# Kernel tuning notes

Measured on AMD Instinct MI355X. Metric: run time of the kernel, lower is better.

## Reference

```python
import jax, jax.numpy as jnp
import numpy as np

DIM = 1024
HEADS = 16
HEAD_DIM = DIM // HEADS
HIDDEN = 4 * DIM
EPS = 1e-5

def _layernorm(x, w, b):
    mu = jnp.mean(x, axis=-1, keepdims=True)
    var = jnp.mean(jnp.square(x - mu), axis=-1, keepdims=True)
    return (x - mu) * jax.lax.rsqrt(var + EPS) * w + b

def setup_inputs() -> dict:
    key = jax.random.key(0)
    ks = jax.random.split(key, 8)
    B, N, C = 4, 1024, DIM
    s = lambda fan_in: 1.0 / np.sqrt(fan_in)
    return {
        "x": jax.random.normal(ks[0], (B, N, C), dtype=jnp.float32),
        "ln1_w": jnp.ones((C,), jnp.float32),
        "ln1_b": jnp.zeros((C,), jnp.float32),
        "qkv_w": jax.random.normal(ks[1], (3 * C, C), jnp.float32) * s(C),
        "proj_w": jax.random.normal(ks[2], (C, C), jnp.float32) * s(C),
        "proj_b": jnp.zeros((C,), jnp.float32),
        "ln2_w": jnp.ones((C,), jnp.float32),
        "ln2_b": jnp.zeros((C,), jnp.float32),
        "fc1_w": jax.random.normal(ks[3], (HIDDEN, C), jnp.float32) * s(C),
        "fc1_b": jnp.zeros((HIDDEN,), jnp.float32),
        "fc2_w": jax.random.normal(ks[4], (C, HIDDEN), jnp.float32) * s(HIDDEN),
        "fc2_b": jnp.zeros((C,), jnp.float32),
    }

def reference(x, ln1_w, ln1_b, qkv_w, proj_w, proj_b, ln2_w, ln2_b, fc1_w, fc1_b, fc2_w, fc2_b):
    B, N, C = x.shape
    H, D = HEADS, HEAD_DIM
    scale = D ** -0.5
    # --- attention branch (pre-norm) ---
    h = _layernorm(x, ln1_w, ln1_b)
    qkv = jnp.einsum('bnc,oc->bno', h, qkv_w)          # [B,N,3C], no bias (qkv_bias=False)
    qkv = qkv.reshape(B, N, 3, H, D)
    q = jnp.transpose(qkv[:, :, 0], (0, 2, 1, 3))       # [B,H,N,D]
    k = jnp.transpose(qkv[:, :, 1], (0, 2, 1, 3))
    v = jnp.transpose(qkv[:, :, 2], (0, 2, 1, 3))
    attn = jnp.einsum('bhnd,bhmd->bhnm', q, k) * scale  # [B,H,N,N]
    attn = jax.nn.softmax(attn, axis=-1)
    o = jnp.einsum('bhnm,bhmd->bhnd', attn, v)          # [B,H,N,D]
    o = jnp.transpose(o, (0, 2, 1, 3)).reshape(B, N, C)
    o = jnp.einsum('bnc,oc->bno', o, proj_w) + proj_b
    x = x + o
    # --- MLP branch (pre-norm); drop=0.0 -> identity ---
    h = _layernorm(x, ln2_w, ln2_b)
    h = jnp.einsum('bnc,hc->bnh', h, fc1_w) + fc1_b
    h = jax.nn.gelu(h, approximate=False)               # nn.GELU exact erf form
    h = jnp.einsum('bnh,ch->bnc', h, fc2_w) + fc2_b
    return x + h
```

## Files before the change

### kernel.cpp

```cpp
#include <hip/hip_runtime.h>
#include <hip/hip_bf16.h>
#include <math.h>
#include <stdint.h>

#define SEQ 1024
#define CDIM 1024
#define NHEAD 16
#define HIDDEN 4096
#define BATCH 4
#define MROWS (BATCH*SEQ)

using bf16x8 = __attribute__((ext_vector_type(8))) short;
using f32x4  = __attribute__((ext_vector_type(4))) float;

__device__ __forceinline__ short f2bf(float f) {
    union { float f; uint32_t u; } c; c.f = f;
    const uint32_t u = c.u + 0x7FFFu + ((c.u >> 16) & 1u);
    return (short)(u >> 16);
}

__device__ __forceinline__ float gelu_exact(float v) {
    return 0.5f * v * (1.0f + erff(v * 0.70710678118654752440f));
}

__device__ __forceinline__ void gload_lds16(const short* g, short* lds) {
    __builtin_amdgcn_global_load_lds(
        (const __attribute__((address_space(1))) void*)(uintptr_t)g,
        (__attribute__((address_space(3))) void*)(uintptr_t)lds,
        16, 0, 0);
}

__global__ void cvt_bf16_kernel(const float* __restrict__ in, short* __restrict__ out) {
    const size_t i = ((size_t)blockIdx.x * 256 + threadIdx.x) * 8;
    const float4 a = *(const float4*)(in + i);
    const float4 b = *(const float4*)(in + i + 4);
    bf16x8 s;
    s[0] = f2bf(a.x); s[1] = f2bf(a.y); s[2] = f2bf(a.z); s[3] = f2bf(a.w);
    s[4] = f2bf(b.x); s[5] = f2bf(b.y); s[6] = f2bf(b.z); s[7] = f2bf(b.w);
    *(bf16x8*)(out + i) = s;
}

__global__ void ln_kernel(const float* __restrict__ x, const float* __restrict__ w,
                          const float* __restrict__ b, short* __restrict__ out) {
    const int row = blockIdx.x;
    const int t = threadIdx.x;
    const float4* xr = (const float4*)(x + (size_t)row * CDIM);
    float4 v = xr[t];
    float s  = v.x + v.y + v.z + v.w;
    float sq = v.x*v.x + v.y*v.y + v.z*v.z + v.w*v.w;
    #pragma unroll
    for (int off = 32; off; off >>= 1) {
        s  += __shfl_down(s, off);
        sq += __shfl_down(sq, off);
    }
    __shared__ float ss[4], ssq[4];
    const int wid = t >> 6, lane = t & 63;
    if (lane == 0) { ss[wid] = s; ssq[wid] = sq; }
    __syncthreads();
    s  = ss[0] + ss[1] + ss[2] + ss[3];
    sq = ssq[0] + ssq[1] + ssq[2] + ssq[3];
    const float mu  = s * (1.0f / CDIM);
    const float var = sq * (1.0f / CDIM) - mu * mu;
    const float rs  = rsqrtf(var + 1e-5f);
    const float4 wv = ((const float4*)w)[t];
    const float4 bv = ((const float4*)b)[t];
    short4 o;
    o.x = f2bf((v.x - mu) * rs * wv.x + bv.x);
    o.y = f2bf((v.y - mu) * rs * wv.y + bv.y);
    o.z = f2bf((v.z - mu) * rs * wv.z + bv.z);
    o.w = f2bf((v.w - mu) * rs * wv.w + bv.w);
    *(short4*)(out + (size_t)row * CDIM + t * 4) = o;
}

template<int BN, bool BIAS, bool RES, bool GELU_, bool OUTBF16>
__global__ __launch_bounds__(256) void mgemm(
    const short* __restrict__ A, const short* __restrict__ B,
    const float* __restrict__ bias, const float* __restrict__ res,
    void* __restrict__ Cv, int M, int N, int K)
{
    constexpr int MF = (BN == 128) ? 4 : 2;
    __shared__ __align__(16) short As[2][128 * 32];
    __shared__ __align__(16) short Bs[2][BN * 32];
    const int t = threadIdx.x;
    const int w = t >> 6, l = t & 63;

    const int gx = gridDim.x;
    const int nwg = gx * gridDim.y;
    const int lid = blockIdx.y * gx + blockIdx.x;
    const int swz = (lid & 7) * (nwg >> 3) + (lid >> 3);
    const int bx = swz % gx, by = swz / gx;
    const int m0 = by * 128, n0 = bx * BN;

    const int wrow = (BN == 128) ? (w >> 1) * 64 : w * 32;
    const int wcol = (BN == 128) ? (w & 1) * 64 : 0;

    const short* agp0 = A + (size_t)(m0 + w * 32 + (l >> 2)) * K + (l & 3) * 8;
    const short* agp1 = agp0 + (size_t)16 * K;
    const short* bgp0;
    const short* bgp1 = nullptr;
    if (BN == 128) {
        bgp0 = B + (size_t)(n0 + w * 32 + (l >> 2)) * K + (l & 3) * 8;
        bgp1 = bgp0 + (size_t)16 * K;
    } else {
        bgp0 = B + (size_t)(n0 + w * 16 + (l >> 2)) * K + (l & 3) * 8;
    }

    int aoff[MF], boff[4];
    #pragma unroll
    for (int m = 0; m < MF; ++m) aoff[m] = (wrow + m * 16 + (l & 15)) * 32 + (l >> 4) * 8;
    #pragma unroll
    for (int n = 0; n < 4; ++n)  boff[n] = (wcol + n * 16 + (l & 15)) * 32 + (l >> 4) * 8;

    auto stage = [&](int k0, int buf) {
        short* ldsA = &As[buf][w * 1024];
        gload_lds16(agp0 + k0, ldsA);
        gload_lds16(agp1 + k0, ldsA + 512);
        if (BN == 128) {
            short* ldsB = &Bs[buf][w * 1024];
            gload_lds16(bgp0 + k0, ldsB);
            gload_lds16(bgp1 + k0, ldsB + 512);
        } else {
            gload_lds16(bgp0 + k0, &Bs[buf][w * 512]);
        }
    };

    f32x4 acc[MF][4] = {};
    stage(0, 0);
    int cur = 0;
    for (int k0 = 0; k0 < K; k0 += 32) {
        __syncthreads();
        if (k0 + 32 < K) stage(k0 + 32, cur ^ 1);
        bf16x8 af[MF], bfr[4];
        #pragma unroll
        for (int m = 0; m < MF; ++m) af[m]  = *(const bf16x8*)&As[cur][aoff[m]];
        #pragma unroll
        for (int n = 0; n < 4; ++n)  bfr[n] = *(const bf16x8*)&Bs[cur][boff[n]];
        #pragma unroll
        for (int m = 0; m < MF; ++m)
            #pragma unroll
            for (int n = 0; n < 4; ++n)
                acc[m][n] = __builtin_amdgcn_mfma_f32_16x16x32_bf16(af[m], bfr[n], acc[m][n], 0, 0, 0);
        cur ^= 1;
    }

    const int lr4 = (l >> 4) * 4, lc = l & 15;
    #pragma unroll
    for (int m = 0; m < MF; ++m) {
        #pragma unroll
        for (int n = 0; n < 4; ++n) {
            const int col = n0 + wcol + n * 16 + lc;
            const float bv = BIAS ? bias[col] : 0.0f;
            #pragma unroll
            for (int r = 0; r < 4; ++r) {
                const int row = m0 + wrow + m * 16 + lr4 + r;
                float v = acc[m][n][r] + bv;
                if (GELU_) v = gelu_exact(v);
                if (RES)   v += res[(size_t)row * N + col];
                if (OUTBF16) ((short*)Cv)[(size_t)row * N + col] = f2bf(v);
                else         ((float*)Cv)[(size_t)row * N + col] = v;
            }
        }
    }
}

__global__ __launch_bounds__(256) void qkv_gemm(
    const short* __restrict__ A, const short* __restrict__ B,
    short* __restrict__ qkvb, short* __restrict__ VT, int K)
{
    __shared__ __align__(16) short As[2][128 * 32];
    __shared__ __align__(16) short Bs[2][128 * 32];
    const int t = threadIdx.x;
    const int w = t >> 6, l = t & 63;
    const int wr = w >> 1, wc = w & 1;

    const int gx = gridDim.x;
    const int nwg = gx * gridDim.y;
    const int lid = blockIdx.y * gx + blockIdx.x;
    const int swz = (lid & 7) * (nwg >> 3) + (lid >> 3);
    const int bx = swz % gx, by = swz / gx;
    const int m0 = by * 128, n0 = bx * 128;

    const short* agp0 = A + (size_t)(m0 + w * 32 + (l >> 2)) * K + (l & 3) * 8;
    const short* agp1 = agp0 + (size_t)16 * K;
    const short* bgp0 = B + (size_t)(n0 + w * 32 + (l >> 2)) * K + (l & 3) * 8;
    const short* bgp1 = bgp0 + (size_t)16 * K;

    int aoff[4], boff[4];
    #pragma unroll
    for (int m = 0; m < 4; ++m) aoff[m] = (wr * 64 + m * 16 + (l & 15)) * 32 + (l >> 4) * 8;
    #pragma unroll
    for (int n = 0; n < 4; ++n) boff[n] = (wc * 64 + n * 16 + (l & 15)) * 32 + (l >> 4) * 8;

    auto stage = [&](int k0, int buf) {
        short* ldsA = &As[buf][w * 1024];
        short* ldsB = &Bs[buf][w * 1024];
        gload_lds16(agp0 + k0, ldsA);
        gload_lds16(agp1 + k0, ldsA + 512);
        gload_lds16(bgp0 + k0, ldsB);
        gload_lds16(bgp1 + k0, ldsB + 512);
    };

    f32x4 acc[4][4] = {};
    stage(0, 0);
    int cur = 0;
    for (int k0 = 0; k0 < K; k0 += 32) {
        __syncthreads();
        if (k0 + 32 < K) stage(k0 + 32, cur ^ 1);
        bf16x8 af[4], bfr[4];
        #pragma unroll
        for (int m = 0; m < 4; ++m) af[m]  = *(const bf16x8*)&As[cur][aoff[m]];
        #pragma unroll
        for (int n = 0; n < 4; ++n) bfr[n] = *(const bf16x8*)&Bs[cur][boff[n]];
        #pragma unroll
        for (int m = 0; m < 4; ++m)
            #pragma unroll
            for (int n = 0; n < 4; ++n)
                acc[m][n] = __builtin_amdgcn_mfma_f32_16x16x32_bf16(af[m], bfr[n], acc[m][n], 0, 0, 0);
        cur ^= 1;
    }

    const int lr4 = (l >> 4) * 4, lc = l & 15;
    if (n0 < 2048) {
        const float sc = (n0 < 1024) ? 0.125f : 1.0f;
        #pragma unroll
        for (int m = 0; m < 4; ++m) {
            #pragma unroll
            for (int n = 0; n < 4; ++n) {
                const int col = n0 + wc * 64 + n * 16 + lc;
                #pragma unroll
                for (int r = 0; r < 4; ++r) {
                    const int row = m0 + wr * 64 + m * 16 + lr4 + r;
                    qkvb[(size_t)row * 2048 + col] = f2bf(acc[m][n][r] * sc);
                }
            }
        }
    } else {
        #pragma unroll
        for (int m = 0; m < 4; ++m) {
            const int row0 = m0 + wr * 64 + m * 16 + lr4;
            const int b = row0 >> 10, nseq = row0 & 1023;
            #pragma unroll
            for (int n = 0; n < 4; ++n) {
                const int c2 = n0 - 2048 + wc * 64 + n * 16 + lc;
                const int h = c2 >> 6, d = c2 & 63;
                short4 v4;
                v4.x = f2bf(acc[m][n][0]); v4.y = f2bf(acc[m][n][1]);
                v4.z = f2bf(acc[m][n][2]); v4.w = f2bf(acc[m][n][3]);
                *(short4*)&VT[(((size_t)(b * 16 + h) * 64 + d) * 1024) + nseq] = v4;
            }
        }
    }
}

__global__ __launch_bounds__(256) void fattn(const short* __restrict__ qkvb,
                                             const short* __restrict__ VT,
                                             short* __restrict__ o) {
    const int bh = blockIdx.y;
    const int b = bh >> 4, h = bh & 15;
    const int q0 = blockIdx.x * 64;
    const int t = threadIdx.x, w = t >> 6, l = t & 63;

    __shared__ __align__(16) short Ks[2][64 * 64];
    __shared__ __align__(16) short Vs[2][64 * 64];
    __shared__ __align__(16) short Ps[4][1024];

    const size_t qrow = (size_t)(b * SEQ + q0 + w * 16 + (l & 15)) * 2048 + h * 64;
    bf16x8 qf[2];
    qf[0] = *(const bf16x8*)&qkvb[qrow + (l >> 4) * 8];
    qf[1] = *(const bf16x8*)&qkvb[qrow + 32 + (l >> 4) * 8];

    const int srow = l >> 3;
    const int sc16 = (l & 7) ^ (srow & 7);
    const short* Kg = qkvb + 1024 + h * 64;
    const short* Vg = VT + (size_t)bh * 64 * 1024;

    f32x4 acc[4] = {};
    float mrow[4] = {-1e30f, -1e30f, -1e30f, -1e30f};
    float lrow[4] = {0.f, 0.f, 0.f, 0.f};

    auto stage = [&](int kt, int buf) {
        const int kv0 = kt * 64;
        #pragma unroll
        for (int i = 0; i < 2; ++i) {
            const int r0 = w * 16 + i * 8;
            gload_lds16(Kg + (size_t)(b * SEQ + kv0 + r0 + srow) * 2048 + sc16 * 8,
                        &Ks[buf][r0 * 64]);
            gload_lds16(Vg + (size_t)(r0 + srow) * 1024 + kv0 + sc16 * 8,
                        &Vs[buf][r0 * 64]);
        }
    };

    stage(0, 0);
    for (int kt = 0; kt < 16; ++kt) {
        const int cur = kt & 1;
        __syncthreads();
        if (kt + 1 < 16) stage(kt + 1, cur ^ 1);

        f32x4 sacc[4];
        #pragma unroll
        for (int nt = 0; nt < 4; ++nt) {
            f32x4 z = {};
            #pragma unroll
            for (int ks = 0; ks < 2; ++ks) {
                const int row = nt * 16 + (l & 15);
                const int c16 = (ks * 4 + (l >> 4)) ^ (row & 7);
                const bf16x8 kf = *(const bf16x8*)&Ks[cur][row * 64 + c16 * 8];
                z = __builtin_amdgcn_mfma_f32_16x16x32_bf16(qf[ks], kf, z, 0, 0, 0);
            }
            sacc[nt] = z;
        }
        float tmax[4], tsum[4], fac[4];
        #pragma unroll
        for (int r = 0; r < 4; ++r)
            tmax[r] = fmaxf(fmaxf(sacc[0][r], sacc[1][r]), fmaxf(sacc[2][r], sacc[3][r]));
        #pragma unroll
        for (int off = 1; off <= 8; off <<= 1)
            #pragma unroll
            for (int r = 0; r < 4; ++r)
                tmax[r] = fmaxf(tmax[r], __shfl_xor(tmax[r], off));
        #pragma unroll
        for (int r = 0; r < 4; ++r) {
            const float nm = fmaxf(mrow[r], tmax[r]);
            fac[r] = __expf(mrow[r] - nm);
            mrow[r] = nm;
            tsum[r] = 0.0f;
        }
        #pragma unroll
        for (int nt = 0; nt < 4; ++nt) {
            #pragma unroll
            for (int r = 0; r < 4; ++r) {
                const float p = __expf(sacc[nt][r] - mrow[r]);
                tsum[r] += p;
                const int q = (l >> 4) * 4 + r;
                const int kv = nt * 16 + (l & 15);
                union { float f; uint32_t u; } cu; cu.f = p;
                Ps[w][q * 64 + (kv ^ ((q & 7) << 3))] = (short)((cu.u + 0x8000u) >> 16);
            }
        }
        #pragma unroll
        for (int off = 1; off <= 8; off <<= 1)
            #pragma unroll
            for (int r = 0; r < 4; ++r)
                tsum[r] += __shfl_xor(tsum[r], off);
        #pragma unroll
        for (int r = 0; r < 4; ++r) lrow[r] = lrow[r] * fac[r] + tsum[r];
        #pragma unroll
        for (int nt2 = 0; nt2 < 4; ++nt2)
            #pragma unroll
            for (int r = 0; r < 4; ++r)
                acc[nt2][r] *= fac[r];
        #pragma unroll
        for (int ks = 0; ks < 2; ++ks) {
            const int ql = l & 15;
            const bf16x8 pa = *(const bf16x8*)&Ps[w][ql * 64 + ((ks * 32 + (l >> 4) * 8) ^ ((ql & 7) << 3))];
            #pragma unroll
            for (int nt2 = 0; nt2 < 4; ++nt2) {
                const int row = nt2 * 16 + (l & 15);
                const int c16 = (ks * 4 + (l >> 4)) ^ (row & 7);
                const bf16x8 vf = *(const bf16x8*)&Vs[cur][row * 64 + c16 * 8];
                acc[nt2] = __builtin_amdgcn_mfma_f32_16x16x32_bf16(pa, vf, acc[nt2], 0, 0, 0);
            }
        }
    }
    #pragma unroll
    for (int r = 0; r < 4; ++r) {
        const float rcp = 1.0f / lrow[r];
        const int q = q0 + w * 16 + (l >> 4) * 4 + r;
        #pragma unroll
        for (int nt2 = 0; nt2 < 4; ++nt2) {
            const int d = nt2 * 16 + (l & 15);
            o[(size_t)(b * SEQ + q) * CDIM + h * 64 + d] = f2bf(acc[nt2][r] * rcp);
        }
    }
}

extern "C" void kernel_launch(void* const* d_in, const int* in_sizes, int n_in,
                              void* d_out, int out_size, void* d_ws, size_t ws_size,
                              hipStream_t stream) {
    const float* x      = (const float*)d_in[0];
    const float* ln1_w  = (const float*)d_in[1];
    const float* ln1_b  = (const float*)d_in[2];
    const float* qkv_w  = (const float*)d_in[3];
    const float* proj_w = (const float*)d_in[4];
    const float* proj_b = (const float*)d_in[5];
    const float* ln2_w  = (const float*)d_in[6];
    const float* ln2_b  = (const float*)d_in[7];
    const float* fc1_w  = (const float*)d_in[8];
    const float* fc1_b  = (const float*)d_in[9];
    const float* fc2_w  = (const float*)d_in[10];
    const float* fc2_b  = (const float*)d_in[11];
    float* out = (float*)d_out;

    short* ws16  = (short*)d_ws;
    short* wqkv  = ws16;
    short* wproj = ws16 + 3145728;
    short* wfc1  = ws16 + 4194304;
    short* wfc2  = ws16 + 8388608;
    char*  wsb   = (char*)d_ws;
    short* qkvb  = (short*)(wsb + (size_t)24 * 1024 * 1024);
    short* VT    = (short*)(wsb + (size_t)40 * 1024 * 1024);
    short* mlp1  = (short*)(wsb + (size_t)24 * 1024 * 1024);
    short* hbuf  = (short*)(wsb + (size_t)72 * 1024 * 1024);

    cvt_bf16_kernel<<<1536, 256, 0, stream>>>(qkv_w, wqkv);
    cvt_bf16_kernel<<< 512, 256, 0, stream>>>(proj_w, wproj);
    cvt_bf16_kernel<<<2048, 256, 0, stream>>>(fc1_w, wfc1);
    cvt_bf16_kernel<<<2048, 256, 0, stream>>>(fc2_w, wfc2);

    ln_kernel<<<MROWS, 256, 0, stream>>>(x, ln1_w, ln1_b, hbuf);
    qkv_gemm<<<dim3(24, 32), 256, 0, stream>>>(hbuf, wqkv, qkvb, VT, 1024);
    fattn<<<dim3(SEQ / 64, BATCH * NHEAD), 256, 0, stream>>>(qkvb, VT, hbuf);
    mgemm<64,true,true,false,false><<<dim3(16, 32), 256, 0, stream>>>(
        hbuf, wproj, proj_b, x, out, MROWS, 1024, 1024);
    ln_kernel<<<MROWS, 256, 0, stream>>>(out, ln2_w, ln2_b, hbuf);
    mgemm<128,true,false,true,true><<<dim3(32, 32), 256, 0, stream>>>(
        hbuf, wfc1, fc1_b, nullptr, mlp1, MROWS, 4096, 1024);
    mgemm<64,true,true,false,false><<<dim3(16, 32), 256, 0, stream>>>(
        mlp1, wfc2, fc2_b, out, out, MROWS, 1024, 4096);
}
```

Measured before the change: 261.6 us.

## Triple-buffer LDS in GEMM kernels with explicit vmcnt waits

Changes the generic GEMM and the QKV GEMM from double to triple LDS buffering. Two k-tiles are prefetched ahead, and each iteration waits on a partial s_waitcnt vmcnt count plus a raw s_barrier instead of a full __syncthreads. This lets global-to-LDS loads overlap more with MFMA work and avoids draining every outstanding load each iteration. In exchange it uses 1.5x the LDS, which may reduce occupancy, and it relies on hand-counted vmcnt values matching the number of loads issued per stage.

```diff
diff --git a/kernel.cpp b/kernel.cpp
--- a/kernel.cpp
+++ b/kernel.cpp
@@ -79,8 +79,8 @@
     void* __restrict__ Cv, int M, int N, int K)
 {
     constexpr int MF = (BN == 128) ? 4 : 2;
-    __shared__ __align__(16) short As[2][128 * 32];
-    __shared__ __align__(16) short Bs[2][BN * 32];
+    __shared__ __align__(16) short As[3][128 * 32];
+    __shared__ __align__(16) short Bs[3][BN * 32];
     const int t = threadIdx.x;
     const int w = t >> 6, l = t & 63;
 
@@ -125,11 +125,24 @@
     };
 
     f32x4 acc[MF][4] = {};
+    const int T = K / 32;
     stage(0, 0);
+    stage(32, 1);
     int cur = 0;
-    for (int k0 = 0; k0 < K; k0 += 32) {
-        __syncthreads();
-        if (k0 + 32 < K) stage(k0 + 32, cur ^ 1);
+    for (int kt = 0; kt < T; ++kt) {
+        if (kt < T - 1) {
+            if constexpr (BN == 128) asm volatile("s_waitcnt vmcnt(4)" ::: "memory");
+            else                     asm volatile("s_waitcnt vmcnt(3)" ::: "memory");
+        } else {
+            asm volatile("s_waitcnt vmcnt(0)" ::: "memory");
+        }
+        __builtin_amdgcn_sched_barrier(0);
+        __builtin_amdgcn_s_barrier();
+        __builtin_amdgcn_sched_barrier(0);
+        if (kt + 2 < T) {
+            int nb = kt + 2; nb -= (nb >= 3) ? ((nb / 3) * 3) : 0;
+            stage((kt + 2) * 32, nb);
+        }
         bf16x8 af[MF], bfr[4];
         #pragma unroll
         for (int m = 0; m < MF; ++m) af[m]  = *(const bf16x8*)&As[cur][aoff[m]];
@@ -140,7 +153,7 @@
             #pragma unroll
             for (int n = 0; n < 4; ++n)
                 acc[m][n] = __builtin_amdgcn_mfma_f32_16x16x32_bf16(af[m], bfr[n], acc[m][n], 0, 0, 0);
-        cur ^= 1;
+        cur = (cur == 2) ? 0 : cur + 1;
     }
 
     const int lr4 = (l >> 4) * 4, lc = l & 15;
@@ -167,8 +180,8 @@
     const short* __restrict__ A, const short* __restrict__ B,
     short* __restrict__ qkvb, short* __restrict__ VT, int K)
 {
-    __shared__ __align__(16) short As[2][128 * 32];
-    __shared__ __align__(16) short Bs[2][128 * 32];
+    __shared__ __align__(16) short As[3][128 * 32];
+    __shared__ __align__(16) short Bs[3][128 * 32];
     const int t = threadIdx.x;
     const int w = t >> 6, l = t & 63;
     const int wr = w >> 1, wc = w & 1;
@@ -201,11 +214,20 @@
     };
 
     f32x4 acc[4][4] = {};
+    const int T = K / 32;
     stage(0, 0);
+    stage(32, 1);
     int cur = 0;
-    for (int k0 = 0; k0 < K; k0 += 32) {
-        __syncthreads();
-        if (k0 + 32 < K) stage(k0 + 32, cur ^ 1);
+    for (int kt = 0; kt < T; ++kt) {
+        if (kt < T - 1) asm volatile("s_waitcnt vmcnt(4)" ::: "memory");
+        else            asm volatile("s_waitcnt vmcnt(0)" ::: "memory");
+        __builtin_amdgcn_sched_barrier(0);
+        __builtin_amdgcn_s_barrier();
+        __builtin_amdgcn_sched_barrier(0);
+        if (kt + 2 < T) {
+            int nb = kt + 2; nb -= (nb >= 3) ? ((nb / 3) * 3) : 0;
+            stage((kt + 2) * 32, nb);
+        }
         bf16x8 af[4], bfr[4];
         #pragma unroll
         for (int m = 0; m < 4; ++m) af[m]  = *(const bf16x8*)&As[cur][aoff[m]];
@@ -216,7 +238,7 @@
             #pragma unroll
             for (int n = 0; n < 4; ++n)
                 acc[m][n] = __builtin_amdgcn_mfma_f32_16x16x32_bf16(af[m], bfr[n], acc[m][n], 0, 0, 0);
-        cur ^= 1;
+        cur = (cur == 2) ? 0 : cur + 1;
     }
 
     const int lr4 = (l >> 4) * 4, lc = l & 15;
```

After: 252.1 us. 1.04x faster.
